# Performance work log

Hardware: AMD Instinct MI355X
Metric: run time of the kernel (lower is better)

## Reference

```python
import jax, jax.numpy as jnp
import numpy as np

# dims: B scenes, V views, T tokens per view, D=d1=d2 embed dim, H=4*D mlp hidden
B, V, T, D = 2, 8, 512, 1024
H = 4 * D
LN_EPS = 1e-5


def setup_inputs() -> dict:
    key = jax.random.key(0)
    ks = jax.random.split(key, 9)
    x = jax.random.normal(ks[0], (B, V, T, D), jnp.float32)
    theta_Q = jax.random.normal(ks[1], (D, D), jnp.float32)  # Task.theta_Q ~ randn
    # TTT_MLP params (nn.Linear default-init scale approximated; exact dist irrelevant for math)
    W1 = jax.random.normal(ks[2], (D, H), jnp.float32) * (1.0 / np.sqrt(D))
    b1 = jnp.zeros((H,), jnp.float32)
    W2 = jax.random.normal(ks[3], (H, D), jnp.float32) * (1.0 / np.sqrt(H))
    b2 = jnp.zeros((D,), jnp.float32)
    gamma = jnp.ones((D,), jnp.float32)   # LayerNorm weight
    beta = jnp.zeros((D,), jnp.float32)   # LayerNorm bias
    alpha = jnp.full((1, D), 0.01, jnp.float32)
    return {"x": x, "theta_Q": theta_Q, "W1": W1, "b1": b1, "W2": W2,
            "b2": b2, "gamma": gamma, "beta": beta, "alpha": alpha}


def _layernorm(y, gamma, beta):
    mu = jnp.mean(y, axis=-1, keepdims=True)
    var = jnp.mean(jnp.square(y - mu), axis=-1, keepdims=True)  # biased, as torch LayerNorm
    return (y - mu) * jax.lax.rsqrt(var + LN_EPS) * gamma + beta


def reference(x, theta_Q, W1, b1, W2, b2, gamma, beta, alpha):
    # NOTE: in the original module, update_model rebinds a local (`p = p - lr*g`),
    # so the learner params are NEVER updated; proxy_loss/grads are dead code w.r.t.
    # the output. Faithful math: out = TTT_MLP(x @ theta_Q), fully parallel over tokens.
    z = jnp.einsum('bvtd,de->bvte', x, theta_Q)          # [B,V,T,D]
    h = jax.nn.gelu(z @ W1 + b1, approximate=False)      # exact erf GELU, as torch nn.GELU
    y = h @ W2 + b2                                      # [B,V,T,D]
    ln = _layernorm(y, gamma, beta)
    return z + jnp.tanh(alpha) * ln
```

## Files before the change

kernel.cpp:

```cpp
#include <hip/hip_runtime.h>
#include <hip/hip_bf16.h>
#include <cstdint>
#include <math.h>

typedef __hip_bfloat16 bf16_t;
typedef __attribute__((ext_vector_type(8))) __bf16 bf16x8;
typedef __attribute__((ext_vector_type(4))) float f32x4;

static_assert(sizeof(bf16x8) == 16, "bf16x8 must be 4 VGPRs");

static constexpr int DD = 1024;
static constexpr int HH = 4096;

#define GLD16(gp, lp)                                                                              \
  __builtin_amdgcn_global_load_lds(                                                                \
      (__attribute__((address_space(1))) void*)(uintptr_t)(gp),                                    \
      (__attribute__((address_space(3))) void*)(uint32_t)(uintptr_t)(lp), 16, 0, 0)

#if !__has_builtin(__builtin_amdgcn_exp2f)
#define __builtin_amdgcn_exp2f(x) exp2f(x)
#endif
#if !__has_builtin(__builtin_amdgcn_rcpf)
#define __builtin_amdgcn_rcpf(x) (1.0f / (x))
#endif

__device__ __forceinline__ float fast_gelu(float u) {
  const float t = __builtin_amdgcn_exp2f(-2.4554089f * u);
  return u * __builtin_amdgcn_rcpf(1.0f + t);
}

__global__ __launch_bounds__(256) void k_split_x(const float* __restrict__ x,
                                                 bf16_t* __restrict__ xh,
                                                 bf16_t* __restrict__ xl, int n4) {
  int i = blockIdx.x * 256 + threadIdx.x;
  const int stride = gridDim.x * 256;
  for (; i < n4; i += stride) {
    const float4 v = reinterpret_cast<const float4*>(x)[i];
    float vv[4] = {v.x, v.y, v.z, v.w};
    union { bf16_t b[4]; short4 s; } H, L;
#pragma unroll
    for (int j = 0; j < 4; ++j) {
      H.b[j] = __float2bfloat16(vv[j]);
      L.b[j] = __float2bfloat16(vv[j] - __bfloat162float(H.b[j]));
    }
    reinterpret_cast<short4*>(xh)[i] = H.s;
    reinterpret_cast<short4*>(xl)[i] = L.s;
  }
}

template <bool SPLIT>
__global__ __launch_bounds__(256) void k_transpose(const float* __restrict__ W,
                                                   bf16_t* __restrict__ Th,
                                                   bf16_t* __restrict__ Tl, int K, int N) {
  __shared__ float tile[32][33];
  const int n0 = blockIdx.x * 32, k0 = blockIdx.y * 32;
  const int tx = threadIdx.x, ty = threadIdx.y;
#pragma unroll
  for (int r = 0; r < 4; ++r) {
    const int k = ty + r * 8;
    tile[k][tx] = W[(size_t)(k0 + k) * N + n0 + tx];
  }
  __syncthreads();
#pragma unroll
  for (int r = 0; r < 4; ++r) {
    const int n = ty + r * 8;
    const float v = tile[tx][n];
    const bf16_t h = __float2bfloat16(v);
    Th[(size_t)(n0 + n) * K + k0 + tx] = h;
    if (SPLIT) Tl[(size_t)(n0 + n) * K + k0 + tx] = __float2bfloat16(v - __bfloat162float(h));
  }
}

template <int EPI, bool SPLIT, int BK>
__global__ __launch_bounds__(256) void k_gemm(const bf16_t* __restrict__ Ah,
                                              const bf16_t* __restrict__ Al,
                                              const bf16_t* __restrict__ BTh,
                                              const bf16_t* __restrict__ BTl,
                                              const float* __restrict__ bias,
                                              float* __restrict__ Cf,
                                              bf16_t* __restrict__ Cb,
                                              int M, int N, int K, int LDK) {
  static_assert(!SPLIT || BK == 32, "SPLIT path only implemented for BK=32");
  constexpr int BM = 128, BN = 128;
  __shared__ __align__(16) bf16_t sAh[BM * BK];
  __shared__ __align__(16) bf16_t sBh[BN * BK];
  __shared__ __align__(16) bf16_t sAl[SPLIT ? BM * BK : 8];
  __shared__ __align__(16) bf16_t sBl[SPLIT ? BN * BK : 8];

  const int nbn = N / BN;
  const int nwg = gridDim.x;
  const int wg = blockIdx.x;
  const int cpx = nwg >> 3;
  const int swz = (wg & 7) * cpx + (wg >> 3);
  const int bm = swz / nbn, bn = swz % nbn;

  const int ks = blockIdx.y;
  const size_t k0 = (size_t)ks * K;
  Cf += (size_t)ks * M * N;

  const int t = threadIdx.x;
  const int l = t & 63;
  const int w = t >> 6;
  const int wr = (w >> 1) * 64, wc = (w & 1) * 64;

  const size_t Abase = (size_t)bm * BM * LDK + k0;
  const size_t Bbase = (size_t)bn * BN * LDK + k0;

  f32x4 acc[4][4] = {};
  const int lm = l & 15;
  const int l4 = l >> 4;

  const int nk = K / BK;
  for (int kt = 0; kt < nk; ++kt) {
    const size_t gk = (size_t)kt * BK;
    if (BK == 32) {
      const int r0 = t >> 2, kc0 = (t & 3) * 8;
      const int r1 = r0 + 64;
      GLD16(Ah + Abase + (size_t)r0 * LDK + gk + kc0, &sAh[r0 * BK + kc0]);
      GLD16(Ah + Abase + (size_t)r1 * LDK + gk + kc0, &sAh[r1 * BK + kc0]);
      GLD16(BTh + Bbase + (size_t)r0 * LDK + gk + kc0, &sBh[r0 * BK + kc0]);
      GLD16(BTh + Bbase + (size_t)r1 * LDK + gk + kc0, &sBh[r1 * BK + kc0]);
      if (SPLIT) {
        GLD16(Al + Abase + (size_t)r0 * LDK + gk + kc0, &sAl[r0 * BK + kc0]);
        GLD16(Al + Abase + (size_t)r1 * LDK + gk + kc0, &sAl[r1 * BK + kc0]);
        GLD16(BTl + Bbase + (size_t)r0 * LDK + gk + kc0, &sBl[r0 * BK + kc0]);
        GLD16(BTl + Bbase + (size_t)r1 * LDK + gk + kc0, &sBl[r1 * BK + kc0]);
      }
    } else {
#pragma unroll
      for (int p = 0; p < 4; ++p) {
        const int c = t + 256 * p;
        const int r = c >> 3, j = c & 7;
        const int jg = (j ^ (r & 7)) * 8;
        GLD16(Ah + Abase + (size_t)r * LDK + gk + jg, &sAh[c * 8]);
      }
#pragma unroll
      for (int p = 0; p < 4; ++p) {
        const int c = t + 256 * p;
        const int r = c >> 3, j = c & 7;
        const int jg = (j ^ (r & 7)) * 8;
        GLD16(BTh + Bbase + (size_t)r * LDK + gk + jg, &sBh[c * 8]);
      }
    }
    __syncthreads();

    if (BK == 32) {
      const int kb8 = l4 * 8;
      bf16x8 a[4], b[4];
#pragma unroll
      for (int m = 0; m < 4; ++m)
        a[m] = *reinterpret_cast<const bf16x8*>(&sAh[(wr + m * 16 + lm) * BK + kb8]);
#pragma unroll
      for (int n = 0; n < 4; ++n)
        b[n] = *reinterpret_cast<const bf16x8*>(&sBh[(wc + n * 16 + lm) * BK + kb8]);
#pragma unroll
      for (int m = 0; m < 4; ++m)
#pragma unroll
        for (int n = 0; n < 4; ++n)
          acc[m][n] = __builtin_amdgcn_mfma_f32_16x16x32_bf16(a[m], b[n], acc[m][n], 0, 0, 0);

      if (SPLIT) {
        bf16x8 al_[4], bl_[4];
#pragma unroll
        for (int m = 0; m < 4; ++m)
          al_[m] = *reinterpret_cast<const bf16x8*>(&sAl[(wr + m * 16 + lm) * BK + kb8]);
#pragma unroll
        for (int n = 0; n < 4; ++n)
          bl_[n] = *reinterpret_cast<const bf16x8*>(&sBl[(wc + n * 16 + lm) * BK + kb8]);
#pragma unroll
        for (int m = 0; m < 4; ++m)
#pragma unroll
          for (int n = 0; n < 4; ++n) {
            acc[m][n] = __builtin_amdgcn_mfma_f32_16x16x32_bf16(a[m], bl_[n], acc[m][n], 0, 0, 0);
            acc[m][n] = __builtin_amdgcn_mfma_f32_16x16x32_bf16(al_[m], b[n], acc[m][n], 0, 0, 0);
          }
      }
    } else {
#pragma unroll
      for (int h = 0; h < 2; ++h) {
        bf16x8 a[4], b[4];
#pragma unroll
        for (int m = 0; m < 4; ++m) {
          const int R = wr + m * 16 + lm;
          const int q = (l4 + 4 * h) ^ (R & 7);
          a[m] = *reinterpret_cast<const bf16x8*>(&sAh[R * 64 + q * 8]);
        }
#pragma unroll
        for (int n = 0; n < 4; ++n) {
          const int R = wc + n * 16 + lm;
          const int q = (l4 + 4 * h) ^ (R & 7);
          b[n] = *reinterpret_cast<const bf16x8*>(&sBh[R * 64 + q * 8]);
        }
#pragma unroll
        for (int m = 0; m < 4; ++m)
#pragma unroll
          for (int n = 0; n < 4; ++n)
            acc[m][n] = __builtin_amdgcn_mfma_f32_16x16x32_bf16(a[m], b[n], acc[m][n], 0, 0, 0);
      }
    }
    __syncthreads();
  }

  const int cr = l4 * 4;
#pragma unroll
  for (int m = 0; m < 4; ++m) {
#pragma unroll
    for (int n = 0; n < 4; ++n) {
      const int c = bn * BN + wc + n * 16 + lm;
      const float bc = (EPI == 2) ? bias[c] : 0.0f;
#pragma unroll
      for (int j = 0; j < 4; ++j) {
        const int r = bm * BM + wr + m * 16 + cr + j;
        const size_t idx = (size_t)r * N + c;
        const float v = acc[m][n][j];
        if (EPI == 1) {
          Cf[idx] = v;
          Cb[idx] = __float2bfloat16(v);
        } else if (EPI == 2) {
          Cb[idx] = __float2bfloat16(fast_gelu(v + bc));
        } else {
          Cf[idx] = v;
        }
      }
    }
  }
}

__global__ __launch_bounds__(256) void k_ln_res(const float* __restrict__ y0,
                                                const float* __restrict__ y1,
                                                const float* __restrict__ b2,
                                                const float* __restrict__ z,
                                                const float* __restrict__ gamma,
                                                const float* __restrict__ beta,
                                                const float* __restrict__ alpha,
                                                float* __restrict__ out) {
  const int row = blockIdx.x;
  const int t = threadIdx.x;
  const float4 va = reinterpret_cast<const float4*>(y0 + (size_t)row * DD)[t];
  const float4 vb = reinterpret_cast<const float4*>(y1 + (size_t)row * DD)[t];
  const float4 bc = reinterpret_cast<const float4*>(b2)[t];
  float4 v;
  v.x = va.x + vb.x + bc.x; v.y = va.y + vb.y + bc.y;
  v.z = va.z + vb.z + bc.z; v.w = va.w + vb.w + bc.w;
  float s = v.x + v.y + v.z + v.w;
  float q = v.x * v.x + v.y * v.y + v.z * v.z + v.w * v.w;
#pragma unroll
  for (int m = 1; m < 64; m <<= 1) {
    s += __shfl_xor(s, m, 64);
    q += __shfl_xor(q, m, 64);
  }
  __shared__ float ss[4], sq[4];
  if ((t & 63) == 0) { ss[t >> 6] = s; sq[t >> 6] = q; }
  __syncthreads();
  s = ss[0] + ss[1] + ss[2] + ss[3];
  q = sq[0] + sq[1] + sq[2] + sq[3];
  const float mu = s * (1.0f / DD);
  const float var = fmaxf(q * (1.0f / DD) - mu * mu, 0.0f);
  const float rs = rsqrtf(var + 1e-5f);
  const float4 g = reinterpret_cast<const float4*>(gamma)[t];
  const float4 bb = reinterpret_cast<const float4*>(beta)[t];
  const float4 aa = reinterpret_cast<const float4*>(alpha)[t];
  const float4 zz = reinterpret_cast<const float4*>(z + (size_t)row * DD)[t];
  float4 o;
  o.x = zz.x + tanhf(aa.x) * ((v.x - mu) * rs * g.x + bb.x);
  o.y = zz.y + tanhf(aa.y) * ((v.y - mu) * rs * g.y + bb.y);
  o.z = zz.z + tanhf(aa.z) * ((v.z - mu) * rs * g.z + bb.z);
  o.w = zz.w + tanhf(aa.w) * ((v.w - mu) * rs * g.w + bb.w);
  reinterpret_cast<float4*>(out + (size_t)row * DD)[t] = o;
}

extern "C" void kernel_launch(void* const* d_in, const int* in_sizes, int n_in, void* d_out,
                              int out_size, void* d_ws, size_t ws_size, hipStream_t stream) {
  const float* x   = (const float*)d_in[0];
  const float* thQ = (const float*)d_in[1];
  const float* W1  = (const float*)d_in[2];
  const float* b1  = (const float*)d_in[3];
  const float* W2  = (const float*)d_in[4];
  const float* b2  = (const float*)d_in[5];
  const float* gam = (const float*)d_in[6];
  const float* bet = (const float*)d_in[7];
  const float* alp = (const float*)d_in[8];
  float* out = (float*)d_out;

  const int M = in_sizes[0] / DD;

  char* ws = (char*)d_ws;
  size_t off = 0;
  auto take = [&](size_t bytes) -> char* {
    char* p = ws + off;
    off += (bytes + 255) & ~(size_t)255;
    return p;
  };
  bf16_t* xh  = (bf16_t*)take((size_t)M * DD * 2);
  bf16_t* xl  = (bf16_t*)take((size_t)M * DD * 2);
  bf16_t* qTh = (bf16_t*)take((size_t)DD * DD * 2);
  bf16_t* qTl = (bf16_t*)take((size_t)DD * DD * 2);
  bf16_t* w1T = (bf16_t*)take((size_t)DD * HH * 2);
  bf16_t* w2T = (bf16_t*)take((size_t)HH * DD * 2);
  float*  zf  = (float*)take((size_t)M * DD * 4);
  bf16_t* zb  = (bf16_t*)take((size_t)M * DD * 2);
  bf16_t* hb  = (bf16_t*)take((size_t)M * HH * 2);
  float*  yf  = (float*)take((size_t)M * DD * 4 * 2);

  hipLaunchKernelGGL(k_split_x, dim3(2048), dim3(256), 0, stream, x, xh, xl, M * DD / 4);
  hipLaunchKernelGGL((k_transpose<true>), dim3(DD / 32, DD / 32), dim3(32, 8), 0, stream,
                     thQ, qTh, qTl, DD, DD);
  hipLaunchKernelGGL((k_transpose<false>), dim3(HH / 32, DD / 32), dim3(32, 8), 0, stream,
                     W1, w1T, (bf16_t*)nullptr, DD, HH);
  hipLaunchKernelGGL((k_transpose<false>), dim3(DD / 32, HH / 32), dim3(32, 8), 0, stream,
                     W2, w2T, (bf16_t*)nullptr, HH, DD);

  hipLaunchKernelGGL((k_gemm<1, true, 32>), dim3((M / 128) * (DD / 128)), dim3(256), 0, stream,
                     xh, xl, qTh, qTl, (const float*)nullptr, zf, zb, M, DD, DD, DD);
  hipLaunchKernelGGL((k_gemm<2, false, 64>), dim3((M / 128) * (HH / 128)), dim3(256), 0, stream,
                     zb, (const bf16_t*)nullptr, w1T, (const bf16_t*)nullptr, b1,
                     (float*)nullptr, hb, M, HH, DD, DD);
  hipLaunchKernelGGL((k_gemm<3, false, 64>), dim3((M / 128) * (DD / 128), 2), dim3(256), 0,
                     stream, hb, (const bf16_t*)nullptr, w2T, (const bf16_t*)nullptr,
                     (const float*)nullptr, yf, (bf16_t*)nullptr, M, DD, HH / 2, HH);
  hipLaunchKernelGGL(k_ln_res, dim3(M), dim3(256), 0, stream,
                     yf, yf + (size_t)M * DD, b2, zf, gam, bet, alp, out);
}
```

Baseline: 389.8 us.

## Double-buffer LDS in BK=64 GEMMs to overlap global loads with MFMA

Splits the templated GEMM into a dedicated split-precision kernel and a new double-buffered kernel for the two large bf16 GEMMs. The pipelined kernel prefetches the next two K-tiles with global_load_lds into alternating LDS buffers, gated by vmcnt waits and explicit barriers, so memory latency overlaps MFMA compute. LDS use doubles to 64 KB per block, which may lower occupancy, and the hand-written waitcnt sequencing must be exactly right for correctness.

Result: faster. 364.0 us (-6.6%).

```diff
diff --git a/kernel.cpp b/kernel.cpp
--- a/kernel.cpp
+++ b/kernel.cpp
@@ -71,21 +71,18 @@
   }
 }
 
-template <int EPI, bool SPLIT, int BK>
-__global__ __launch_bounds__(256) void k_gemm(const bf16_t* __restrict__ Ah,
-                                              const bf16_t* __restrict__ Al,
-                                              const bf16_t* __restrict__ BTh,
-                                              const bf16_t* __restrict__ BTl,
-                                              const float* __restrict__ bias,
-                                              float* __restrict__ Cf,
-                                              bf16_t* __restrict__ Cb,
-                                              int M, int N, int K, int LDK) {
-  static_assert(!SPLIT || BK == 32, "SPLIT path only implemented for BK=32");
-  constexpr int BM = 128, BN = 128;
+__global__ __launch_bounds__(256) void k_gemm_split(const bf16_t* __restrict__ Ah,
+                                                    const bf16_t* __restrict__ Al,
+                                                    const bf16_t* __restrict__ BTh,
+                                                    const bf16_t* __restrict__ BTl,
+                                                    float* __restrict__ Cf,
+                                                    bf16_t* __restrict__ Cb,
+                                                    int M, int N, int K) {
+  constexpr int BM = 128, BN = 128, BK = 32;
   __shared__ __align__(16) bf16_t sAh[BM * BK];
   __shared__ __align__(16) bf16_t sBh[BN * BK];
-  __shared__ __align__(16) bf16_t sAl[SPLIT ? BM * BK : 8];
-  __shared__ __align__(16) bf16_t sBl[SPLIT ? BN * BK : 8];
+  __shared__ __align__(16) bf16_t sAl[BM * BK];
+  __shared__ __align__(16) bf16_t sBl[BN * BK];
 
   const int nbn = N / BN;
   const int nwg = gridDim.x;
@@ -94,109 +91,63 @@
   const int swz = (wg & 7) * cpx + (wg >> 3);
   const int bm = swz / nbn, bn = swz % nbn;
 
-  const int ks = blockIdx.y;
-  const size_t k0 = (size_t)ks * K;
-  Cf += (size_t)ks * M * N;
-
   const int t = threadIdx.x;
   const int l = t & 63;
   const int w = t >> 6;
   const int wr = (w >> 1) * 64, wc = (w & 1) * 64;
 
-  const size_t Abase = (size_t)bm * BM * LDK + k0;
-  const size_t Bbase = (size_t)bn * BN * LDK + k0;
+  const size_t Abase = (size_t)bm * BM * K;
+  const size_t Bbase = (size_t)bn * BN * K;
+
+  const int r0 = t >> 2, kc0 = (t & 3) * 8;
+  const int r1 = r0 + 64;
 
   f32x4 acc[4][4] = {};
   const int lm = l & 15;
   const int l4 = l >> 4;
+  const int kb8 = l4 * 8;
 
   const int nk = K / BK;
   for (int kt = 0; kt < nk; ++kt) {
     const size_t gk = (size_t)kt * BK;
-    if (BK == 32) {
-      const int r0 = t >> 2, kc0 = (t & 3) * 8;
-      const int r1 = r0 + 64;
-      GLD16(Ah + Abase + (size_t)r0 * LDK + gk + kc0, &sAh[r0 * BK + kc0]);
-      GLD16(Ah + Abase + (size_t)r1 * LDK + gk + kc0, &sAh[r1 * BK + kc0]);
-      GLD16(BTh + Bbase + (size_t)r0 * LDK + gk + kc0, &sBh[r0 * BK + kc0]);
-      GLD16(BTh + Bbase + (size_t)r1 * LDK + gk + kc0, &sBh[r1 * BK + kc0]);
-      if (SPLIT) {
-        GLD16(Al + Abase + (size_t)r0 * LDK + gk + kc0, &sAl[r0 * BK + kc0]);
-        GLD16(Al + Abase + (size_t)r1 * LDK + gk + kc0, &sAl[r1 * BK + kc0]);
-        GLD16(BTl + Bbase + (size_t)r0 * LDK + gk + kc0, &sBl[r0 * BK + kc0]);
-        GLD16(BTl + Bbase + (size_t)r1 * LDK + gk + kc0, &sBl[r1 * BK + kc0]);
-      }
-    } else {
-#pragma unroll
-      for (int p = 0; p < 4; ++p) {
-        const int c = t + 256 * p;
-        const int r = c >> 3, j = c & 7;
-        const int jg = (j ^ (r & 7)) * 8;
-        GLD16(Ah + Abase + (size_t)r * LDK + gk + jg, &sAh[c * 8]);
-      }
-#pragma unroll
-      for (int p = 0; p < 4; ++p) {
-        const int c = t + 256 * p;
-        const int r = c >> 3, j = c & 7;
-        const int jg = (j ^ (r & 7)) * 8;
-        GLD16(BTh + Bbase + (size_t)r * LDK + gk + jg, &sBh[c * 8]);
-      }
-    }
+    GLD16(Ah + Abase + (size_t)r0 * K + gk + kc0, &sAh[r0 * BK + kc0]);
+    GLD16(Ah + Abase + (size_t)r1 * K + gk + kc0, &sAh[r1 * BK + kc0]);
+    GLD16(BTh + Bbase + (size_t)r0 * K + gk + kc0, &sBh[r0 * BK + kc0]);
+    GLD16(BTh + Bbase + (size_t)r1 * K + gk + kc0, &sBh[r1 * BK + kc0]);
+    GLD16(Al + Abase + (size_t)r0 * K + gk + kc0, &sAl[r0 * BK + kc0]);
+    GLD16(Al + Abase + (size_t)r1 * K + gk + kc0, &sAl[r1 * BK + kc0]);
+    GLD16(BTl + Bbase + (size_t)r0 * K + gk + kc0, &sBl[r0 * BK + kc0]);
+    GLD16(BTl + Bbase + (size_t)r1 * K + gk + kc0, &sBl[r1 * BK + kc0]);
     __syncthreads();
 
-    if (BK == 32) {
-      const int kb8 = l4 * 8;
-      bf16x8 a[4], b[4];
+    bf16x8 a[4], b[4];
+#pragma unroll
+    for (int m = 0; m < 4; ++m)
+      a[m] = *reinterpret_cast<const bf16x8*>(&sAh[(wr + m * 16 + lm) * BK + kb8]);
+#pragma unroll
+    for (int n = 0; n < 4; ++n)
+      b[n] = *reinterpret_cast<const bf16x8*>(&sBh[(wc + n * 16 + lm) * BK + kb8]);
+#pragma unroll
+    for (int m = 0; m < 4; ++m)
+#pragma unroll
+      for (int n = 0; n < 4; ++n)
+        acc[m][n] = __builtin_amdgcn_mfma_f32_16x16x32_bf16(a[m], b[n], acc[m][n], 0, 0, 0);
+
+    {
+      bf16x8 al_[4], bl_[4];
 #pragma unroll
       for (int m = 0; m < 4; ++m)
-        a[m] = *reinterpret_cast<const bf16x8*>(&sAh[(wr + m * 16 + lm) * BK + kb8]);
+        al_[m] = *reinterpret_cast<const bf16x8*>(&sAl[(wr + m * 16 + lm) * BK + kb8]);
 #pragma unroll
       for (int n = 0; n < 4; ++n)
-        b[n] = *reinterpret_cast<const bf16x8*>(&sBh[(wc + n * 16 + lm) * BK + kb8]);
+        bl_[n] = *reinterpret_cast<const bf16x8*>(&sBl[(wc + n * 16 + lm) * BK + kb8]);
 #pragma unroll
       for (int m = 0; m < 4; ++m)
 #pragma unroll
-        for (int n = 0; n < 4; ++n)
-          acc[m][n] = __builtin_amdgcn_mfma_f32_16x16x32_bf16(a[m], b[n], acc[m][n], 0, 0, 0);
-
-      if (SPLIT) {
-        bf16x8 al_[4], bl_[4];
-#pragma unroll
-        for (int m = 0; m < 4; ++m)
-          al_[m] = *reinterpret_cast<const bf16x8*>(&sAl[(wr + m * 16 + lm) * BK + kb8]);
-#pragma unroll
-        for (int n = 0; n < 4; ++n)
-          bl_[n] = *reinterpret_cast<const bf16x8*>(&sBl[(wc + n * 16 + lm) * BK + kb8]);
-#pragma unroll
-        for (int m = 0; m < 4; ++m)
-#pragma unroll
-          for (int n = 0; n < 4; ++n) {
-            acc[m][n] = __builtin_amdgcn_mfma_f32_16x16x32_bf16(a[m], bl_[n], acc[m][n], 0, 0, 0);
-            acc[m][n] = __builtin_amdgcn_mfma_f32_16x16x32_bf16(al_[m], b[n], acc[m][n], 0, 0, 0);
-          }
-      }
-    } else {
-#pragma unroll
-      for (int h = 0; h < 2; ++h) {
-        bf16x8 a[4], b[4];
-#pragma unroll
-        for (int m = 0; m < 4; ++m) {
-          const int R = wr + m * 16 + lm;
-          const int q = (l4 + 4 * h) ^ (R & 7);
-          a[m] = *reinterpret_cast<const bf16x8*>(&sAh[R * 64 + q * 8]);
+        for (int n = 0; n < 4; ++n) {
+          acc[m][n] = __builtin_amdgcn_mfma_f32_16x16x32_bf16(a[m], bl_[n], acc[m][n], 0, 0, 0);
+          acc[m][n] = __builtin_amdgcn_mfma_f32_16x16x32_bf16(al_[m], b[n], acc[m][n], 0, 0, 0);
         }
-#pragma unroll
-        for (int n = 0; n < 4; ++n) {
-          const int R = wc + n * 16 + lm;
-          const int q = (l4 + 4 * h) ^ (R & 7);
-          b[n] = *reinterpret_cast<const bf16x8*>(&sBh[R * 64 + q * 8]);
-        }
-#pragma unroll
-        for (int m = 0; m < 4; ++m)
-#pragma unroll
-          for (int n = 0; n < 4; ++n)
-            acc[m][n] = __builtin_amdgcn_mfma_f32_16x16x32_bf16(a[m], b[n], acc[m][n], 0, 0, 0);
-      }
     }
     __syncthreads();
   }
@@ -207,16 +158,124 @@
 #pragma unroll
     for (int n = 0; n < 4; ++n) {
       const int c = bn * BN + wc + n * 16 + lm;
-      const float bc = (EPI == 2) ? bias[c] : 0.0f;
 #pragma unroll
       for (int j = 0; j < 4; ++j) {
         const int r = bm * BM + wr + m * 16 + cr + j;
         const size_t idx = (size_t)r * N + c;
         const float v = acc[m][n][j];
-        if (EPI == 1) {
-          Cf[idx] = v;
-          Cb[idx] = __float2bfloat16(v);
-        } else if (EPI == 2) {
+        Cf[idx] = v;
+        Cb[idx] = __float2bfloat16(v);
+      }
+    }
+  }
+}
+
+template <int EPI>
+__global__ __launch_bounds__(256) void k_gemm_pipe(const bf16_t* __restrict__ A,
+                                                   const bf16_t* __restrict__ BT,
+                                                   const float* __restrict__ bias,
+                                                   float* __restrict__ Cf,
+                                                   bf16_t* __restrict__ Cb,
+                                                   int M, int N, int K, int LDK) {
+  constexpr int BM = 128, BN = 128, BK = 64;
+  __shared__ __align__(16) bf16_t sA[2][BM * BK];
+  __shared__ __align__(16) bf16_t sB[2][BN * BK];
+
+  const int nbn = N / BN;
+  const int nwg = gridDim.x;
+  const int wg = blockIdx.x;
+  const int cpx = nwg >> 3;
+  const int swz = (wg & 7) * cpx + (wg >> 3);
+  const int bm = swz / nbn, bn = swz % nbn;
+
+  const int ks = blockIdx.y;
+  const size_t k0 = (size_t)ks * K;
+  Cf += (size_t)ks * M * N;
+
+  const int t = threadIdx.x;
+  const int l = t & 63;
+  const int w = t >> 6;
+  const int wr = (w >> 1) * 64, wc = (w & 1) * 64;
+
+  const size_t Abase = (size_t)bm * BM * LDK + k0;
+  const size_t Bbase = (size_t)bn * BN * LDK + k0;
+
+  const int lm = l & 15;
+  const int l4 = l >> 4;
+
+  auto stage = [&](int kt, int pb) {
+    const size_t gk = (size_t)kt * BK;
+#pragma unroll
+    for (int p = 0; p < 4; ++p) {
+      const int c = t + 256 * p;
+      const int r = c >> 3, j = c & 7;
+      const int jg = (j ^ (r & 7)) * 8;
+      GLD16(A + Abase + (size_t)r * LDK + gk + jg, &sA[pb][c * 8]);
+    }
+#pragma unroll
+    for (int p = 0; p < 4; ++p) {
+      const int c = t + 256 * p;
+      const int r = c >> 3, j = c & 7;
+      const int jg = (j ^ (r & 7)) * 8;
+      GLD16(BT + Bbase + (size_t)r * LDK + gk + jg, &sB[pb][c * 8]);
+    }
+  };
+
+  f32x4 acc[4][4] = {};
+  const int nk = K / BK;
+
+  stage(0, 0);
+  stage(1, 1);
+  for (int kt = 0; kt < nk; ++kt) {
+    const int pb = kt & 1;
+    if (kt + 1 < nk) {
+      asm volatile("s_waitcnt vmcnt(8)" ::: "memory");
+    } else {
+      asm volatile("s_waitcnt vmcnt(0)" ::: "memory");
+    }
+    __builtin_amdgcn_s_barrier();
+    __builtin_amdgcn_sched_barrier(0);
+
+#pragma unroll
+    for (int h = 0; h < 2; ++h) {
+      bf16x8 a[4], b[4];
+#pragma unroll
+      for (int m = 0; m < 4; ++m) {
+        const int R = wr + m * 16 + lm;
+        const int q = (l4 + 4 * h) ^ (R & 7);
+        a[m] = *reinterpret_cast<const bf16x8*>(&sA[pb][R * 64 + q * 8]);
+      }
+#pragma unroll
+      for (int n = 0; n < 4; ++n) {
+        const int R = wc + n * 16 + lm;
+        const int q = (l4 + 4 * h) ^ (R & 7);
+        b[n] = *reinterpret_cast<const bf16x8*>(&sB[pb][R * 64 + q * 8]);
+      }
+#pragma unroll
+      for (int m = 0; m < 4; ++m)
+#pragma unroll
+        for (int n = 0; n < 4; ++n)
+          acc[m][n] = __builtin_amdgcn_mfma_f32_16x16x32_bf16(a[m], b[n], acc[m][n], 0, 0, 0);
+    }
+
+    __builtin_amdgcn_sched_barrier(0);
+    __builtin_amdgcn_s_barrier();
+    if (kt + 2 < nk) stage(kt + 2, pb);
+  }
+
+  const int cr = l4 * 4;
+#pragma unroll
+  for (int m = 0; m < 4; ++m) {
+#pragma unroll
+    for (int n = 0; n < 4; ++n) {
+      const int c = bn * BN + wc + n * 16 + lm;
+      const float bc = (EPI == 2) ? bias[c] : 0.0f;
+#pragma unroll
+      for (int j = 0; j < 4; ++j) {
+        const int r = bm * BM + wr + m * 16 + cr + j;
+        const size_t idx = (size_t)r * N + c;
+        const float v = acc[m][n][j];
+        if (EPI == 2) {
           Cb[idx] = __float2bfloat16(fast_gelu(v + bc));
         } else {
           Cf[idx] = v;
@@ -310,14 +369,12 @@
   hipLaunchKernelGGL((k_transpose<false>), dim3(DD / 32, HH / 32), dim3(32, 8), 0, stream,
                      W2, w2T, (bf16_t*)nullptr, HH, DD);
 
-  hipLaunchKernelGGL((k_gemm<1, true, 32>), dim3((M / 128) * (DD / 128)), dim3(256), 0, stream,
-                     xh, xl, qTh, qTl, (const float*)nullptr, zf, zb, M, DD, DD, DD);
-  hipLaunchKernelGGL((k_gemm<2, false, 64>), dim3((M / 128) * (HH / 128)), dim3(256), 0, stream,
-                     zb, (const bf16_t*)nullptr, w1T, (const bf16_t*)nullptr, b1,
-                     (float*)nullptr, hb, M, HH, DD, DD);
-  hipLaunchKernelGGL((k_gemm<3, false, 64>), dim3((M / 128) * (DD / 128), 2), dim3(256), 0,
-                     stream, hb, (const bf16_t*)nullptr, w2T, (const bf16_t*)nullptr,
-                     (const float*)nullptr, yf, (bf16_t*)nullptr, M, DD, HH / 2, HH);
+  hipLaunchKernelGGL(k_gemm_split, dim3((M / 128) * (DD / 128)), dim3(256), 0, stream,
+                     xh, xl, qTh, qTl, zf, zb, M, DD, DD);
+  hipLaunchKernelGGL((k_gemm_pipe<2>), dim3((M / 128) * (HH / 128)), dim3(256), 0, stream,
+                     zb, w1T, b1, (float*)nullptr, hb, M, HH, DD, DD);
+  hipLaunchKernelGGL((k_gemm_pipe<3>), dim3((M / 128) * (DD / 128), 2), dim3(256), 0, stream,
+                     hb, w2T, (const float*)nullptr, yf, (bf16_t*)nullptr, M, DD, HH / 2, HH);
   hipLaunchKernelGGL(k_ln_res, dim3(M), dim3(256), 0, stream,
                      yf, yf + (size_t)M * DD, b2, zf, gam, bet, alp, out);
 }
```
